# Kernel optimization log

Hardware: AMD Instinct MI355X
Metric: run time of the kernel (lower is better)

Reference implementation:

```python
import jax, jax.numpy as jnp
import numpy as np

C, N_PIX, K = 32, 65536, 8_000_000  # channels, image pixels, correspondence pairs
H, W, D = 128, 128, 64              # Hough voxel grid


def setup_inputs() -> dict:
    key = jax.random.key(0)
    k0, k1, k2, k3, k4 = jax.random.split(key, 5)
    feats_src_dst = jax.random.normal(k0, (C, N_PIX), dtype=jnp.float32)
    voxels_src = jax.random.randint(k1, (K,), 0, H * W * D, dtype=jnp.int32)
    voxels_dst = jax.random.randint(k2, (K,), 0, H * W * D, dtype=jnp.int32)
    idxs_src = jax.random.randint(k3, (K,), 0, N_PIX, dtype=jnp.int32)
    idxs_dst = jax.random.randint(k4, (K,), 0, N_PIX, dtype=jnp.int32)
    return {
        "feats_src_dst": feats_src_dst,
        "voxels_src": voxels_src,
        "voxels_dst": voxels_dst,
        "idxs_src": idxs_src,
        "idxs_dst": idxs_dst,
        "h": H, "w": W, "d": D,
    }


def reference(feats_src_dst, voxels_src, voxels_dst, idxs_src, idxs_dst, h, w, d):
    # Scatter-accumulate gathered pixel features into the Hough voxel volume:
    # vol[c, voxels_src[k]] += feats[c, idxs_src[k]] ; same for dst pairs.
    c = feats_src_dst.shape[0]
    n_vox = h * w * d
    vol = jnp.zeros((c, n_vox), dtype=feats_src_dst.dtype)
    vol = vol.at[:, voxels_src].add(feats_src_dst[:, idxs_src])
    vol = vol.at[:, voxels_dst].add(feats_src_dst[:, idxs_dst])
    return vol.reshape(c, h, w, d)
```

## Files before the change

### kernel.cpp

```cpp
#include <hip/hip_runtime.h>

#define CCH 32
#define NPIX 65536
#define NVOX (1 << 20)
#define NC 256
#define NF 4096
#define VPB 256
#define SCAP 5120
#define EVB1 8192
#define CHK2 8192
#define J2 12

typedef unsigned int u32;

__device__ __forceinline__ u32 f2bf(float x) {
    u32 u = __float_as_uint(x);
    return (u + 0x7FFFu + ((u >> 16) & 1u)) >> 16;
}

__global__ __launch_bounds__(256) void feats_bf_k(
    const float* __restrict__ feats, u32* __restrict__ fbf)
{
    __shared__ float lds[64][33];
    int p0 = blockIdx.x * 64;
    int t = threadIdx.x;
#pragma unroll
    for (int r = 0; r < 8; ++r) {
        int u = r * 256 + t;
        int c = u >> 6, x = u & 63;
        lds[x][c] = feats[(size_t)c * NPIX + p0 + x];
    }
    __syncthreads();
#pragma unroll
    for (int r = 0; r < 4; ++r) {
        int w = r * 256 + t;
        int pix = w >> 4, cp = w & 15;
        u32 lo = f2bf(lds[pix][2 * cp]);
        u32 hi = f2bf(lds[pix][2 * cp + 1]);
        fbf[((size_t)(p0 + pix) << 4) + cp] = lo | (hi << 16);
    }
}

__global__ __launch_bounds__(512) void hist1_k(
    const int* __restrict__ vs, const int* __restrict__ vd, int K,
    u32* __restrict__ hist1)
{
    __shared__ u32 h[NC];
    int t = threadIdx.x;
    if (t < NC) h[t] = 0;
    __syncthreads();
    int total = 2 * K;
    int e0 = blockIdx.x * EVB1, e1 = min(e0 + EVB1, total);
    if ((e1 <= K || e0 >= K) && (e1 - e0) == EVB1) {
        const int4* v4 = (const int4*)((e0 < K) ? vs + e0 : vd + (e0 - K));
#pragma unroll
        for (int r = 0; r < 4; ++r) {
            int4 v = v4[t + r * 512];
            atomicAdd(&h[((u32)v.x) >> 12], 1u);
            atomicAdd(&h[((u32)v.y) >> 12], 1u);
            atomicAdd(&h[((u32)v.z) >> 12], 1u);
            atomicAdd(&h[((u32)v.w) >> 12], 1u);
        }
    } else {
        for (int e = e0 + t; e < e1; e += 512) {
            u32 v = (u32)((e < K) ? vs[e] : vd[e - K]);
            atomicAdd(&h[v >> 12], 1u);
        }
    }
    __syncthreads();
    if (t < NC) hist1[(size_t)blockIdx.x * NC + t] = h[t];
}

__global__ __launch_bounds__(256) void scanA_k(
    u32* __restrict__ hist1, int nblk, u32* __restrict__ coarseTot)
{
    __shared__ u32 s[256];
    int bin = blockIdx.x, t = threadIdx.x;
    int P = (nblk + 255) >> 8;
    u32 c[8];
    u32 sum = 0;
#pragma unroll
    for (int r = 0; r < 8; ++r) {
        int j = t * P + r;
        c[r] = (r < P && j < nblk) ? hist1[(size_t)j * NC + bin] : 0u;
        sum += c[r];
    }
    s[t] = sum;
    __syncthreads();
    u32 incl = sum;
    for (int d = 1; d < 256; d <<= 1) {
        u32 x = (t >= d) ? s[t - d] : 0u;
        __syncthreads();
        incl += x; s[t] = incl;
        __syncthreads();
    }
    u32 excl = incl - sum;
#pragma unroll
    for (int r = 0; r < 8; ++r) {
        int j = t * P + r;
        if (r < P && j < nblk) hist1[(size_t)j * NC + bin] = excl;
        excl += c[r];
    }
    if (t == 255) coarseTot[bin] = incl;
}

__global__ __launch_bounds__(256) void scanB_k(
    const u32* __restrict__ coarseTot, u32* __restrict__ coarseBase)
{
    __shared__ u32 s[256];
    int t = threadIdx.x;
    u32 v = coarseTot[t];
    s[t] = v;
    __syncthreads();
    u32 incl = v;
    for (int d = 1; d < 256; d <<= 1) {
        u32 x = (t >= d) ? s[t - d] : 0u;
        __syncthreads();
        incl += x; s[t] = incl;
        __syncthreads();
    }
    coarseBase[t] = incl - v;
    if (t == 255) coarseBase[256] = incl;
}

__global__ __launch_bounds__(512) void scatter1_k(
    const int* __restrict__ vs, const int* __restrict__ vd,
    const int* __restrict__ is_, const int* __restrict__ id_, int K,
    const u32* __restrict__ hist1, const u32* __restrict__ coarseBase,
    u32* __restrict__ binned1)
{
    __shared__ u32 sorted[EVB1];
    __shared__ u32 hst[NC];
    __shared__ u32 sc[NC];
    __shared__ u32 cur[NC];
    __shared__ u32 st[NC + 1];
    __shared__ u32 gb[NC];

    int t = threadIdx.x;
    if (t < NC) {
        hst[t] = 0;
        gb[t] = coarseBase[t] + hist1[(size_t)blockIdx.x * NC + t];
    }
    __syncthreads();

    int total = 2 * K;
    int e0 = blockIdx.x * EVB1, e1 = min(e0 + EVB1, total);
    u32 pv[16], cv[16];
    if ((e1 <= K || e0 >= K) && (e1 - e0) == EVB1) {
        const int4* v4 = (const int4*)((e0 < K) ? vs + e0 : vd + (e0 - K));
        const int4* i4 = (const int4*)((e0 < K) ? is_ + e0 : id_ + (e0 - K));
#pragma unroll
        for (int r = 0; r < 4; ++r) {
            int4 v = v4[t + r * 512];
            int4 ii = i4[t + r * 512];
            cv[4 * r + 0] = ((u32)v.x) >> 12; pv[4 * r + 0] = (((u32)v.x & 0xFFFu) << 16) | (u32)ii.x;
            cv[4 * r + 1] = ((u32)v.y) >> 12; pv[4 * r + 1] = (((u32)v.y & 0xFFFu) << 16) | (u32)ii.y;
            cv[4 * r + 2] = ((u32)v.z) >> 12; pv[4 * r + 2] = (((u32)v.z & 0xFFFu) << 16) | (u32)ii.z;
            cv[4 * r + 3] = ((u32)v.w) >> 12; pv[4 * r + 3] = (((u32)v.w & 0xFFFu) << 16) | (u32)ii.w;
            atomicAdd(&hst[cv[4 * r + 0]], 1u);
            atomicAdd(&hst[cv[4 * r + 1]], 1u);
            atomicAdd(&hst[cv[4 * r + 2]], 1u);
            atomicAdd(&hst[cv[4 * r + 3]], 1u);
        }
    } else {
#pragma unroll
        for (int r = 0; r < 16; ++r) {
            int e = e0 + t + r * 512;
            cv[r] = 0xFFFFFFFFu;
            if (e < e1) {
                u32 v, i;
                if (e < K) { v = (u32)vs[e];     i = (u32)is_[e]; }
                else       { v = (u32)vd[e - K]; i = (u32)id_[e - K]; }
                cv[r] = v >> 12;
                pv[r] = ((v & 0xFFFu) << 16) | i;
                atomicAdd(&hst[cv[r]], 1u);
            }
        }
    }
    __syncthreads();

    if (t < NC) sc[t] = hst[t];
    __syncthreads();
    for (int d = 1; d < NC; d <<= 1) {
        u32 x = 0;
        if (t < NC && t >= d) x = sc[t - d];
        __syncthreads();
        if (t < NC) sc[t] += x;
        __syncthreads();
    }
    if (t < NC) { u32 ex = sc[t] - hst[t]; st[t] = ex; cur[t] = ex; }
    if (t == 0) st[NC] = (u32)(e1 - e0);
    __syncthreads();

#pragma unroll
    for (int r = 0; r < 16; ++r) {
        if (cv[r] != 0xFFFFFFFFu) {
            u32 pos = atomicAdd(&cur[cv[r]], 1u);
            sorted[pos] = pv[r];
        }
    }
    __syncthreads();

    int w = t >> 6, lane = t & 63;
    for (int cb = w * 32; cb < w * 32 + 32; ++cb) {
        u32 s0 = st[cb], cnt = st[cb + 1] - s0;
        u32 g0 = gb[cb];
        for (u32 u = lane; u < cnt; u += 64)
            binned1[(size_t)g0 + u] = sorted[s0 + u];
    }
}

__global__ __launch_bounds__(256) void hist2_k(
    const u32* __restrict__ binned1, const u32* __restrict__ coarseBase,
    u32* __restrict__ hist2)
{
    __shared__ u32 h[16];
    int c = blockIdx.x / J2, j = blockIdx.x % J2;
    int t = threadIdx.x;
    if (t < 16) h[t] = 0;
    __syncthreads();
    u32 cb0 = coarseBase[c], cb1 = coarseBase[c + 1];
    u32 w0 = cb0 + (u32)j * CHK2;
    u32 w1 = min(w0 + (u32)CHK2, cb1);
    for (u32 e = w0 + t; e < w1; e += 256)
        atomicAdd(&h[(binned1[e] >> 24) & 15u], 1u);
    __syncthreads();
    if (t < 16) hist2[(size_t)blockIdx.x * 16 + t] = h[t];
}

__global__ __launch_bounds__(256) void scan2_k(
    const u32* __restrict__ hist2, const u32* __restrict__ coarseBase,
    u32* __restrict__ cfBase, u32* __restrict__ fineBase)
{
    __shared__ u32 jex[J2 * 16];
    __shared__ u32 ftot[16];
    __shared__ u32 fex[16];
    int c = blockIdx.x, t = threadIdx.x;
    if (t < 16) {
        u32 run = 0;
        for (int j = 0; j < J2; ++j) {
            jex[j * 16 + t] = run;
            run += hist2[((size_t)c * J2 + j) * 16 + t];
        }
        ftot[t] = run;
    }
    __syncthreads();
    if (t == 0) {
        u32 r = coarseBase[c];
        for (int f = 0; f < 16; ++f) { fex[f] = r; r += ftot[f]; }
    }
    __syncthreads();
    if (t < 16) fineBase[c * 16 + t] = fex[t];
    for (int u = t; u < J2 * 16; u += 256) {
        int j = u >> 4, f = u & 15;
        cfBase[((size_t)c * J2 + j) * 16 + f] = fex[f] + jex[u];
    }
    if (c == NC - 1 && t == 0) fineBase[NF] = coarseBase[NC];
}

__global__ __launch_bounds__(512) void scatter2_k(
    const u32* __restrict__ binned1, const u32* __restrict__ coarseBase,
    const u32* __restrict__ cfBase, u32* __restrict__ binned2)
{
    __shared__ u32 sorted[CHK2];
    __shared__ u32 hst[16], st[17], cur[16], gb[16];
    int c = blockIdx.x / J2, j = blockIdx.x % J2;
    int t = threadIdx.x;
    u32 cb0 = coarseBase[c], cb1 = coarseBase[c + 1];
    u32 w0 = cb0 + (u32)j * CHK2;
    u32 w1 = min(w0 + (u32)CHK2, cb1);
    if (w0 >= w1) return;
    if (t < 16) { hst[t] = 0; gb[t] = cfBase[((size_t)c * J2 + j) * 16 + t]; }
    __syncthreads();
    int n = (int)(w1 - w0);
    u32 pv[16], fv[16];
#pragma unroll
    for (int r = 0; r < 16; ++r) {
        int e = t + r * 512;
        fv[r] = 0xFFFFFFFFu;
        if (e < n) {
            u32 p = binned1[w0 + e];
            pv[r] = p;
            fv[r] = (p >> 24) & 15u;
            atomicAdd(&hst[fv[r]], 1u);
        }
    }
    __syncthreads();
    if (t == 0) {
        u32 r = 0;
        for (int f = 0; f < 16; ++f) { st[f] = r; r += hst[f]; }
        st[16] = r;
    }
    __syncthreads();
    if (t < 16) cur[t] = st[t];
    __syncthreads();
#pragma unroll
    for (int r = 0; r < 16; ++r) {
        if (fv[r] != 0xFFFFFFFFu) {
            u32 pos = atomicAdd(&cur[fv[r]], 1u);
            sorted[pos] = pv[r] & 0x00FFFFFFu;
        }
    }
    __syncthreads();
    int w = t >> 6, lane = t & 63;
    for (int f = w * 2; f < w * 2 + 2; ++f) {
        u32 s0 = st[f], cnt = st[f + 1] - s0, g0 = gb[f];
        for (u32 u = lane; u < cnt; u += 64)
            binned2[(size_t)g0 + u] = sorted[s0 + u];
    }
}

__global__ __launch_bounds__(1024) void accum_k(
    const u32* __restrict__ fbf, const u32* __restrict__ binned2,
    const u32* __restrict__ fineBase, float* __restrict__ out)
{
    __shared__ unsigned short sorted[SCAP + 32];
    __shared__ float tile[VPB][33];
    __shared__ u32 hist[VPB];
    __shared__ u32 cursor[VPB];
    __shared__ u32 voff[VPB + 1];

    int t = threadIdx.x;
    int b = blockIdx.x;
    u32 start = fineBase[b];
    int cnt = (int)min(fineBase[b + 1] - start, (u32)SCAP);
    const u32* bp = binned2 + start;

    if (t < VPB) hist[t] = 0;
    __syncthreads();

    u32 p0_ = 0, p1_ = 0, p2_ = 0, p3_ = 0, p4_ = 0;
    bool n0 = t < cnt, n1 = t + 1024 < cnt, n2 = t + 2048 < cnt,
         n3 = t + 3072 < cnt, n4 = t + 4096 < cnt;
    if (n0) { p0_ = bp[t];        atomicAdd(&hist[(p0_ >> 16) & 255u], 1u); }
    if (n1) { p1_ = bp[t + 1024]; atomicAdd(&hist[(p1_ >> 16) & 255u], 1u); }
    if (n2) { p2_ = bp[t + 2048]; atomicAdd(&hist[(p2_ >> 16) & 255u], 1u); }
    if (n3) { p3_ = bp[t + 3072]; atomicAdd(&hist[(p3_ >> 16) & 255u], 1u); }
    if (n4) { p4_ = bp[t + 4096]; atomicAdd(&hist[(p4_ >> 16) & 255u], 1u); }
    __syncthreads();

    if (t < 64) {
        u32 h0 = hist[4 * t], h1 = hist[4 * t + 1],
            h2 = hist[4 * t + 2], h3 = hist[4 * t + 3];
        u32 lsum = h0 + h1 + h2 + h3;
        u32 run = lsum;
#pragma unroll
        for (int d = 1; d < 64; d <<= 1) {
            u32 x = __shfl_up(run, d, 64);
            if (t >= d) run += x;
        }
        u32 e = run - lsum;
        voff[4 * t] = e;                  cursor[4 * t] = e;
        voff[4 * t + 1] = e + h0;         cursor[4 * t + 1] = e + h0;
        voff[4 * t + 2] = e + h0 + h1;    cursor[4 * t + 2] = e + h0 + h1;
        voff[4 * t + 3] = e + h0 + h1 + h2; cursor[4 * t + 3] = e + h0 + h1 + h2;
        if (t == 63) voff[VPB] = (u32)cnt;
    }
    __syncthreads();

    if (n0) { u32 pos = atomicAdd(&cursor[(p0_ >> 16) & 255u], 1u); sorted[pos] = (unsigned short)p0_; }
    if (n1) { u32 pos = atomicAdd(&cursor[(p1_ >> 16) & 255u], 1u); sorted[pos] = (unsigned short)p1_; }
    if (n2) { u32 pos = atomicAdd(&cursor[(p2_ >> 16) & 255u], 1u); sorted[pos] = (unsigned short)p2_; }
    if (n3) { u32 pos = atomicAdd(&cursor[(p3_ >> 16) & 255u], 1u); sorted[pos] = (unsigned short)p3_; }
    if (n4) { u32 pos = atomicAdd(&cursor[(p4_ >> 16) & 255u], 1u); sorted[pos] = (unsigned short)p4_; }
    __syncthreads();

    const uint4* f4 = (const uint4*)fbf;
    int wave = t >> 6, lane = t & 63;
    int chq  = lane & 3;
    int grp  = lane >> 2;
    int vb   = (wave << 4) + grp;
    int s  = (int)voff[vb];
    int e2 = (int)voff[vb + 1];

    float a0 = 0.f, a1 = 0.f, a2 = 0.f, a3 = 0.f,
          a4 = 0.f, a5 = 0.f, a6 = 0.f, a7 = 0.f;
#pragma unroll 2
    for (int k = s; k < e2; ++k) {
        u32 idx = sorted[k];
        uint4 w = f4[((size_t)idx << 2) + chq];
        a0 += __uint_as_float(w.x << 16);
        a1 += __uint_as_float(w.x & 0xFFFF0000u);
        a2 += __uint_as_float(w.y << 16);
        a3 += __uint_as_float(w.y & 0xFFFF0000u);
        a4 += __uint_as_float(w.z << 16);
        a5 += __uint_as_float(w.z & 0xFFFF0000u);
        a6 += __uint_as_float(w.w << 16);
        a7 += __uint_as_float(w.w & 0xFFFF0000u);
    }
    int cb = chq * 8;
    tile[vb][cb + 0] = a0; tile[vb][cb + 1] = a1;
    tile[vb][cb + 2] = a2; tile[vb][cb + 3] = a3;
    tile[vb][cb + 4] = a4; tile[vb][cb + 5] = a5;
    tile[vb][cb + 6] = a6; tile[vb][cb + 7] = a7;
    __syncthreads();

    int v0 = b << 8;
    for (int u = t; u < CCH * VPB; u += 1024) {
        int cc = u >> 8, vv = u & 255;
        out[((size_t)cc << 20) + v0 + vv] = tile[vv][cc];
    }
}

__global__ __launch_bounds__(256) void scatter_direct_k(
    const float* __restrict__ feats,
    const int* __restrict__ vox_s, const int* __restrict__ vox_d,
    const int* __restrict__ idx_s, const int* __restrict__ idx_d,
    float* __restrict__ out, int K)
{
    int c = threadIdx.x & 31;
    int g = (blockIdx.x * blockDim.x + threadIdx.x) >> 5;
    int gstride = (gridDim.x * blockDim.x) >> 5;
    int total = 2 * K;
    for (int e = g; e < total; e += gstride) {
        int v, i;
        if (e < K) { v = vox_s[e];     i = idx_s[e]; }
        else       { v = vox_d[e - K]; i = idx_d[e - K]; }
        atomicAdd(&out[(size_t)c * NVOX + v], feats[(size_t)c * NPIX + i]);
    }
}

extern "C" void kernel_launch(void* const* d_in, const int* in_sizes, int n_in,
                              void* d_out, int out_size, void* d_ws, size_t ws_size,
                              hipStream_t stream)
{
    const float* feats = (const float*)d_in[0];
    const int* vox_s   = (const int*)d_in[1];
    const int* vox_d   = (const int*)d_in[2];
    const int* idx_s   = (const int*)d_in[3];
    const int* idx_d   = (const int*)d_in[4];
    const int  K       = in_sizes[1];
    float* out = (float*)d_out;

    const int total = 2 * K;
    const int nblk1 = (total + EVB1 - 1) / EVB1;

    size_t off = 0;
    auto alloc = [&](size_t bytes) {
        size_t o = off; off = (off + bytes + 255) & ~(size_t)255; return o;
    };
    const size_t b1_o  = alloc((size_t)total * 4);
    const size_t b2_o  = alloc((size_t)total * 4 + 256);
    const size_t h1_o  = alloc((size_t)nblk1 * NC * 4);
    const size_t ct_o  = alloc(NC * 4);
    const size_t cb_o  = alloc((NC + 1) * 4);
    const size_t h2_o  = alloc((size_t)NC * J2 * 16 * 4);
    const size_t cf_o  = alloc((size_t)NC * J2 * 16 * 4);
    const size_t fb_o  = alloc((NF + 1) * 4);
    const size_t fbf_o = alloc((size_t)NPIX * 16 * 4);
    const size_t need  = off;

    if (ws_size >= need && nblk1 <= 2048) {
        char* ws = (char*)d_ws;
        u32* binned1    = (u32*)(ws + b1_o);
        u32* binned2    = (u32*)(ws + b2_o);
        u32* hist1      = (u32*)(ws + h1_o);
        u32* coarseTot  = (u32*)(ws + ct_o);
        u32* coarseBase = (u32*)(ws + cb_o);
        u32* hist2      = (u32*)(ws + h2_o);
        u32* cfBase     = (u32*)(ws + cf_o);
        u32* fineBase   = (u32*)(ws + fb_o);
        u32* fbf        = (u32*)(ws + fbf_o);

        feats_bf_k<<<NPIX / 64, 256, 0, stream>>>(feats, fbf);
        hist1_k<<<nblk1, 512, 0, stream>>>(vox_s, vox_d, K, hist1);
        scanA_k<<<NC, 256, 0, stream>>>(hist1, nblk1, coarseTot);
        scanB_k<<<1, 256, 0, stream>>>(coarseTot, coarseBase);
        scatter1_k<<<nblk1, 512, 0, stream>>>(vox_s, vox_d, idx_s, idx_d, K,
                                              hist1, coarseBase, binned1);
        hist2_k<<<NC * J2, 256, 0, stream>>>(binned1, coarseBase, hist2);
        scan2_k<<<NC, 256, 0, stream>>>(hist2, coarseBase, cfBase, fineBase);
        scatter2_k<<<NC * J2, 512, 0, stream>>>(binned1, coarseBase, cfBase, binned2);
        accum_k<<<NF, 1024, 0, stream>>>(fbf, binned2, fineBase, out);
    } else {
        hipMemsetAsync(d_out, 0, (size_t)out_size * sizeof(float), stream);
        scatter_direct_k<<<8192, 256, 0, stream>>>(feats, vox_s, vox_d, idx_s, idx_d, out, K);
    }
}
```

Baseline: 271.7 us.

## Shrink accum_k to 256 threads, four voxels per thread, direct float4 stores

The final accumulation kernel goes from 1024 to 256 threads per block. Each thread now accumulates four consecutive voxels for its eight channels and writes them straight to global memory as float4 stores, so the LDS transpose tile and its barrier are gone. The histogram and local sort loops become strided loops over the bin entries. Lower LDS use and the launch bound are meant to raise occupancy, but there are fewer threads per block to hide gather latency and 32 accumulators per thread raise register pressure.

```diff
diff --git a/kernel.cpp b/kernel.cpp
--- a/kernel.cpp
+++ b/kernel.cpp
@@ -310,12 +310,11 @@
     }
 }
 
-__global__ __launch_bounds__(1024) void accum_k(
+__global__ __launch_bounds__(256, 4) void accum_k(
     const u32* __restrict__ fbf, const u32* __restrict__ binned2,
     const u32* __restrict__ fineBase, float* __restrict__ out)
 {
     __shared__ unsigned short sorted[SCAP + 32];
-    __shared__ float tile[VPB][33];
     __shared__ u32 hist[VPB];
     __shared__ u32 cursor[VPB];
     __shared__ u32 voff[VPB + 1];
@@ -326,17 +325,11 @@
     int cnt = (int)min(fineBase[b + 1] - start, (u32)SCAP);
     const u32* bp = binned2 + start;
 
-    if (t < VPB) hist[t] = 0;
-    __syncthreads();
-
-    u32 p0_ = 0, p1_ = 0, p2_ = 0, p3_ = 0, p4_ = 0;
-    bool n0 = t < cnt, n1 = t + 1024 < cnt, n2 = t + 2048 < cnt,
-         n3 = t + 3072 < cnt, n4 = t + 4096 < cnt;
-    if (n0) { p0_ = bp[t];        atomicAdd(&hist[(p0_ >> 16) & 255u], 1u); }
-    if (n1) { p1_ = bp[t + 1024]; atomicAdd(&hist[(p1_ >> 16) & 255u], 1u); }
-    if (n2) { p2_ = bp[t + 2048]; atomicAdd(&hist[(p2_ >> 16) & 255u], 1u); }
-    if (n3) { p3_ = bp[t + 3072]; atomicAdd(&hist[(p3_ >> 16) & 255u], 1u); }
-    if (n4) { p4_ = bp[t + 4096]; atomicAdd(&hist[(p4_ >> 16) & 255u], 1u); }
+    hist[t] = 0;
+    __syncthreads();
+
+    for (int e = t; e < cnt; e += 256)
+        atomicAdd(&hist[(bp[e] >> 16) & 255u], 1u);
     __syncthreads();
 
     if (t < 64) {
@@ -350,55 +343,56 @@
             if (t >= d) run += x;
         }
         u32 e = run - lsum;
-        voff[4 * t] = e;                  cursor[4 * t] = e;
-        voff[4 * t + 1] = e + h0;         cursor[4 * t + 1] = e + h0;
-        voff[4 * t + 2] = e + h0 + h1;    cursor[4 * t + 2] = e + h0 + h1;
+        voff[4 * t] = e;                    cursor[4 * t] = e;
+        voff[4 * t + 1] = e + h0;           cursor[4 * t + 1] = e + h0;
+        voff[4 * t + 2] = e + h0 + h1;      cursor[4 * t + 2] = e + h0 + h1;
         voff[4 * t + 3] = e + h0 + h1 + h2; cursor[4 * t + 3] = e + h0 + h1 + h2;
         if (t == 63) voff[VPB] = (u32)cnt;
     }
     __syncthreads();
 
-    if (n0) { u32 pos = atomicAdd(&cursor[(p0_ >> 16) & 255u], 1u); sorted[pos] = (unsigned short)p0_; }
-    if (n1) { u32 pos = atomicAdd(&cursor[(p1_ >> 16) & 255u], 1u); sorted[pos] = (unsigned short)p1_; }
-    if (n2) { u32 pos = atomicAdd(&cursor[(p2_ >> 16) & 255u], 1u); sorted[pos] = (unsigned short)p2_; }
-    if (n3) { u32 pos = atomicAdd(&cursor[(p3_ >> 16) & 255u], 1u); sorted[pos] = (unsigned short)p3_; }
-    if (n4) { u32 pos = atomicAdd(&cursor[(p4_ >> 16) & 255u], 1u); sorted[pos] = (unsigned short)p4_; }
+    for (int e = t; e < cnt; e += 256) {
+        u32 p = bp[e];
+        u32 pos = atomicAdd(&cursor[(p >> 16) & 255u], 1u);
+        sorted[pos] = (unsigned short)p;
+    }
     __syncthreads();
 
     const uint4* f4 = (const uint4*)fbf;
-    int wave = t >> 6, lane = t & 63;
-    int chq  = lane & 3;
-    int grp  = lane >> 2;
-    int vb   = (wave << 4) + grp;
-    int s  = (int)voff[vb];
-    int e2 = (int)voff[vb + 1];
-
-    float a0 = 0.f, a1 = 0.f, a2 = 0.f, a3 = 0.f,
-          a4 = 0.f, a5 = 0.f, a6 = 0.f, a7 = 0.f;
+    int chq = t & 3;
+    int g   = t >> 2;
+    int vb0 = g << 2;
+
+    float acc[4][8];
+#pragma unroll
+    for (int v = 0; v < 4; ++v)
+#pragma unroll
+        for (int j = 0; j < 8; ++j) acc[v][j] = 0.f;
+
+#pragma unroll
+    for (int v = 0; v < 4; ++v) {
+        int s  = (int)voff[vb0 + v];
+        int e2 = (int)voff[vb0 + v + 1];
 #pragma unroll 2
-    for (int k = s; k < e2; ++k) {
-        u32 idx = sorted[k];
-        uint4 w = f4[((size_t)idx << 2) + chq];
-        a0 += __uint_as_float(w.x << 16);
-        a1 += __uint_as_float(w.x & 0xFFFF0000u);
-        a2 += __uint_as_float(w.y << 16);
-        a3 += __uint_as_float(w.y & 0xFFFF0000u);
-        a4 += __uint_as_float(w.z << 16);
-        a5 += __uint_as_float(w.z & 0xFFFF0000u);
-        a6 += __uint_as_float(w.w << 16);
-        a7 += __uint_as_float(w.w & 0xFFFF0000u);
-    }
+        for (int k = s; k < e2; ++k) {
+            uint4 w = f4[((size_t)sorted[k] << 2) + chq];
+            acc[v][0] += __uint_as_float(w.x << 16);
+            acc[v][1] += __uint_as_float(w.x & 0xFFFF0000u);
+            acc[v][2] += __uint_as_float(w.y << 16);
+            acc[v][3] += __uint_as_float(w.y & 0xFFFF0000u);
+            acc[v][4] += __uint_as_float(w.z << 16);
+            acc[v][5] += __uint_as_float(w.z & 0xFFFF0000u);
+            acc[v][6] += __uint_as_float(w.w << 16);
+            acc[v][7] += __uint_as_float(w.w & 0xFFFF0000u);
+        }
+    }
+
+    size_t vabs = ((size_t)b << 8) + (size_t)vb0;
     int cb = chq * 8;
-    tile[vb][cb + 0] = a0; tile[vb][cb + 1] = a1;
-    tile[vb][cb + 2] = a2; tile[vb][cb + 3] = a3;
-    tile[vb][cb + 4] = a4; tile[vb][cb + 5] = a5;
-    tile[vb][cb + 6] = a6; tile[vb][cb + 7] = a7;
-    __syncthreads();
-
-    int v0 = b << 8;
-    for (int u = t; u < CCH * VPB; u += 1024) {
-        int cc = u >> 8, vv = u & 255;
-        out[((size_t)cc << 20) + v0 + vv] = tile[vv][cc];
+#pragma unroll
+    for (int j = 0; j < 8; ++j) {
+        float4 stv = make_float4(acc[0][j], acc[1][j], acc[2][j], acc[3][j]);
+        *(float4*)&out[(size_t)(cb + j) * NVOX + vabs] = stv;
     }
 }
 
@@ -471,7 +465,7 @@
         hist2_k<<<NC * J2, 256, 0, stream>>>(binned1, coarseBase, hist2);
         scan2_k<<<NC, 256, 0, stream>>>(hist2, coarseBase, cfBase, fineBase);
         scatter2_k<<<NC * J2, 512, 0, stream>>>(binned1, coarseBase, cfBase, binned2);
-        accum_k<<<NF, 1024, 0, stream>>>(fbf, binned2, fineBase, out);
+        accum_k<<<NF, 256, 0, stream>>>(fbf, binned2, fineBase, out);
     } else {
         hipMemsetAsync(d_out, 0, (size_t)out_size * sizeof(float), stream);
         scatter_direct_k<<<8192, 256, 0, stream>>>(feats, vox_s, vox_d, idx_s, idx_d, out, K);
```

Result: no change. 275.1 us (+1.3%).
